# Optimization experiments

Hardware: AMD Instinct MI355X
Metric: run time of the kernel (lower is better)

## Reference

```python
import jax, jax.numpy as jnp
import numpy as np

J = 24
ROOT = 0
# SMPL kinematic tree parents
PARENTS = [-1, 0, 0, 0, 1, 2, 3, 4, 5, 6, 7, 8, 9, 9, 9, 12, 13, 14, 16, 17, 18, 19, 20, 21]
RES_SCALE = 0.1


def rodrigues(rvec):
    """Axis-angle (..., 3) -> rotation matrix (..., 3, 3)."""
    theta = jnp.linalg.norm(rvec, axis=-1, keepdims=True)          # (...,1)
    axis = rvec / jnp.maximum(theta, 1e-8)
    x, y, z = axis[..., 0], axis[..., 1], axis[..., 2]
    zero = jnp.zeros_like(x)
    K = jnp.stack([zero, -z, y, z, zero, -x, -y, x, zero], axis=-1)
    K = K.reshape(rvec.shape[:-1] + (3, 3))
    s = jnp.sin(theta)[..., None]
    c = jnp.cos(theta)[..., None]
    I = jnp.eye(3, dtype=rvec.dtype)
    return I + s * K + (1.0 - c) * (K @ K)


def _make_T(R, t):
    """(B,3,3),(B,3) -> (B,4,4) homogeneous transform."""
    B = R.shape[0]
    top = jnp.concatenate([R, t[..., None]], axis=-1)              # (B,3,4)
    bottom = jnp.broadcast_to(jnp.array([0., 0., 0., 1.], R.dtype), (B, 1, 4))
    return jnp.concatenate([top, bottom], axis=-2)


def calculate_kinematic(rest_pose, rvecs, root_locs):
    """rest_pose (J,3), rvecs (B,J,3), root_locs (B,3) -> kp (B,J,3), skts (B,J,4,4).
    Sequential tree-structured chain, unrolled over the 24 joints."""
    R = rodrigues(rvecs)                                           # (B,J,3,3)
    B = rvecs.shape[0]
    l2w = [None] * J
    l2w[ROOT] = _make_T(R[:, ROOT], root_locs)
    for j in range(1, J):
        p = PARENTS[j]
        t_local = jnp.broadcast_to(rest_pose[j] - rest_pose[p], (B, 3))
        l2w[j] = l2w[p] @ _make_T(R[:, j], t_local)
    l2w = jnp.stack(l2w, axis=1)                                   # (B,J,4,4)
    kp = l2w[..., :3, 3]                                           # (B,J,3)
    # skts = inverse(l2w) = [R^T, -R^T t]
    Rt = jnp.swapaxes(l2w[..., :3, :3], -1, -2)
    t_inv = -(Rt @ kp[..., None])                                  # (B,J,3,1)
    top = jnp.concatenate([Rt, t_inv], axis=-1)                    # (B,J,3,4)
    bottom = jnp.broadcast_to(jnp.array([0., 0., 0., 1.], l2w.dtype), (B, J, 1, 4))
    skts = jnp.concatenate([top, bottom], axis=-2)                 # (B,J,4,4)
    return kp, skts


def setup_inputs() -> dict:
    key = jax.random.key(0)
    ks = jax.random.split(key, 12)
    N, NU, E, W = 131072, 16384, 16, 128
    skip = N // NU
    din, dout = J * 3 + E, J * 3 + 3
    bones = jax.random.normal(ks[0], (N, J, 3), jnp.float32) * 0.2
    pelvis_buf = jax.random.normal(ks[1], (NU, 3), jnp.float32)
    kp_idxs = jnp.arange(N, dtype=jnp.int64) // skip
    rest_pose = jax.random.normal(ks[2], (J, 3), jnp.float32) * 0.3
    rest_pose = rest_pose.at[ROOT].set(0.0)
    # kp3d root must match pelvis buffer (original asserts allclose)
    kp3d = jnp.zeros((N, J, 3), jnp.float32).at[:, ROOT].set(pelvis_buf[kp_idxs])
    emb_table = jax.random.normal(ks[3], (NU, E), jnp.float32) * 0.02
    def lin(k, fan_in, fan_out):
        lim = 1.0 / np.sqrt(fan_in)
        k1, k2 = jax.random.split(k)
        return (jax.random.uniform(k1, (fan_in, fan_out), jnp.float32, -lim, lim),
                jax.random.uniform(k2, (fan_out,), jnp.float32, -lim, lim))
    W0, b0 = lin(ks[4], din, W)
    W1, b1 = lin(ks[5], W, W)
    W2, b2 = lin(ks[6], W, W)
    W3, b3 = lin(ks[7], W, dout)
    return dict(bones=bones, kp3d=kp3d, kp_idxs=kp_idxs, emb_table=emb_table,
                pelvis_buf=pelvis_buf, rest_pose=rest_pose,
                W0=W0, b0=b0, W1=W1, b1=b1, W2=W2, b2=b2, W3=W3, b3=b3,
                N_unique=NU)


def reference(bones, kp3d, kp_idxs, emb_table, pelvis_buf, rest_pose,
              W0, b0, W1, b1, W2, b2, W3, b3, N_unique):
    N = bones.shape[0]
    skip = N // N_unique
    rvecs = bones[::skip].reshape(N_unique, J * 3)                 # (Nu, 72)
    kp_u = kp_idxs[::skip]
    embs = emb_table[kp_u]                                         # (Nu, 16)
    pelvis = pelvis_buf[kp_u]                                      # (Nu, 3)
    x = jnp.concatenate([rvecs, embs], axis=-1)
    h = jax.nn.relu(x @ W0 + b0)
    h = jax.nn.relu(h @ W1 + b1)
    h = jax.nn.relu(h @ W2 + b2)
    residual = (h @ W3 + b3) * RES_SCALE                           # (Nu, 75)
    rvecs = (rvecs + residual[:, :J * 3]).reshape(N_unique, J, 3)
    pelvis = pelvis + residual[:, J * 3:]
    kp, skts = calculate_kinematic(rest_pose, rvecs, pelvis)
    # expand unique poses back to full batch ('i s ... -> (i s) ...')
    kp = jnp.repeat(kp, skip, axis=0)                              # (N,J,3)
    skts = jnp.repeat(skts, skip, axis=0)                          # (N,J,4,4)
    rvecs = jnp.repeat(rvecs, skip, axis=0)                        # (N,J,3)
    return kp, skts, rvecs
```

## Files before the change

kernel.cpp:

```cpp
#include <hip/hip_runtime.h>
#include <hip/hip_bf16.h>

typedef unsigned short u16;
using f32x4 = __attribute__((ext_vector_type(4))) float;
using s16x8 = __attribute__((ext_vector_type(8))) short;
using u32x4 = __attribute__((ext_vector_type(4))) unsigned int;

#define JNT 24
#define STRX 104
#define STRH 136

__device__ __forceinline__ u16 f2bf(float f) {
    unsigned int x; __builtin_memcpy(&x, &f, 4);
    unsigned int lsb = (x >> 16) & 1u;
    x += 0x7fffu + lsb;
    return (u16)(x >> 16);
}

__global__ void prep_weights(const float* __restrict__ W0, const float* __restrict__ W1,
                             const float* __restrict__ W2, const float* __restrict__ W3,
                             u16* __restrict__ wst) {
    int i = blockIdx.x * 256 + threadIdx.x;
    if (i < 12288) { int n = i / 96, k = i - n * 96; wst[i] = (k < 88) ? f2bf(W0[k * 128 + n]) : (u16)0; return; }
    i -= 12288;
    if (i < 16384) { int n = i >> 7, k = i & 127; wst[12288 + i] = f2bf(W1[k * 128 + n]); return; }
    i -= 16384;
    if (i < 16384) { int n = i >> 7, k = i & 127; wst[28672 + i] = f2bf(W2[k * 128 + n]); return; }
    i -= 16384;
    if (i < 10240) { int n = i >> 7, k = i & 127; wst[45056 + i] = (n < 75) ? f2bf(W3[k * 75 + n]) : (u16)0; }
}

template<int BASE, int CNT>
__device__ __forceinline__ void mlp_l3(const u16* __restrict__ H, const u16* __restrict__ W3t,
                                       const float* __restrict__ b3, float* __restrict__ res_s,
                                       int lr, int lk, int drow) {
    f32x4 acc[CNT];
#pragma unroll
    for (int t = 0; t < CNT; ++t) {
        int col = (BASE + t) * 16 + lr;
        float bv = (col < 75) ? b3[col] : 0.f;
        acc[t] = (f32x4){bv, bv, bv, bv};
    }
#pragma unroll
    for (int ks = 0; ks < 4; ++ks) {
        s16x8 a = *(const s16x8*)&H[lr * STRH + ks * 32 + lk];
#pragma unroll
        for (int t = 0; t < CNT; ++t) {
            s16x8 b = *(const s16x8*)&W3t[((BASE + t) * 16 + lr) * 128 + ks * 32 + lk];
            acc[t] = __builtin_amdgcn_mfma_f32_16x16x32_bf16(a, b, acc[t], 0, 0, 0);
        }
    }
#pragma unroll
    for (int t = 0; t < CNT; ++t) {
        int col = (BASE + t) * 16 + lr;
        if (col < 75) {
#pragma unroll
            for (int q = 0; q < 4; ++q)
                res_s[(drow + q) * 80 + col] = acc[t][q] * 0.1f;
        }
    }
}

__device__ const int KPARP[32] = {0,0,0,0,1,2,3,4,5,6,7,8,9,9,9,12,13,14,16,17,18,19,20,21,0,0,0,0,0,0,0,0};
__device__ const int KDEPP[32] = {0,1,1,1,2,2,2,3,3,3,4,4,4,4,4,5,5,5,6,6,7,7,8,8,99,99,99,99,99,99,99,99};

__global__ __launch_bounds__(256, 3)
void fused_kernel(const float* __restrict__ bones, const float* __restrict__ emb,
                  const float* __restrict__ pelvis, const float* __restrict__ rest,
                  const float* __restrict__ b0, const float* __restrict__ b1,
                  const float* __restrict__ b2, const float* __restrict__ b3,
                  const u16* __restrict__ wst, float* __restrict__ out,
                  int N, int bstride) {
    __shared__ __align__(16) unsigned char smem[22016];
    float* res_s = (float*)smem;
    u16* Xs = (u16*)(smem + 5120);
    u16* H1 = (u16*)(smem + 8448);
    u16* H2 = (u16*)(smem + 12800);
    float* so8 = (float*)(smem + 5120);

    const int tid = threadIdx.x;
    const int row0 = blockIdx.x * 16;

    for (int i = tid; i < 16 * 96; i += 256) {
        int r = i / 96, c = i - r * 96;
        int u = row0 + r;
        float v = 0.f;
        if (c < 72)      v = bones[(size_t)u * bstride + c];
        else if (c < 88) v = emb[(size_t)u * 16 + (c - 72)];
        Xs[r * STRX + c] = f2bf(v);
    }
    __syncthreads();

    const int lane = tid & 63;
    const int wave = tid >> 6;
    const int lr = lane & 15;
    const int lk = (lane >> 4) * 8;
    const int drow = (lane >> 4) * 4;
    const u16* W0t = wst;
    const u16* W1t = wst + 12288;
    const u16* W2t = wst + 28672;
    const u16* W3t = wst + 45056;

    {
        f32x4 acc[2];
#pragma unroll
        for (int t = 0; t < 2; ++t) { float bv = b0[(wave * 2 + t) * 16 + lr]; acc[t] = (f32x4){bv, bv, bv, bv}; }
#pragma unroll
        for (int ks = 0; ks < 3; ++ks) {
            s16x8 a = *(const s16x8*)&Xs[lr * STRX + ks * 32 + lk];
#pragma unroll
            for (int t = 0; t < 2; ++t) {
                s16x8 b = *(const s16x8*)&W0t[((wave * 2 + t) * 16 + lr) * 96 + ks * 32 + lk];
                acc[t] = __builtin_amdgcn_mfma_f32_16x16x32_bf16(a, b, acc[t], 0, 0, 0);
            }
        }
#pragma unroll
        for (int t = 0; t < 2; ++t)
#pragma unroll
            for (int q = 0; q < 4; ++q)
                H1[(drow + q) * STRH + (wave * 2 + t) * 16 + lr] = f2bf(fmaxf(acc[t][q], 0.f));
    }
    __syncthreads();
    {
        f32x4 acc[2];
#pragma unroll
        for (int t = 0; t < 2; ++t) { float bv = b1[(wave * 2 + t) * 16 + lr]; acc[t] = (f32x4){bv, bv, bv, bv}; }
#pragma unroll
        for (int ks = 0; ks < 4; ++ks) {
            s16x8 a = *(const s16x8*)&H1[lr * STRH + ks * 32 + lk];
#pragma unroll
            for (int t = 0; t < 2; ++t) {
                s16x8 b = *(const s16x8*)&W1t[((wave * 2 + t) * 16 + lr) * 128 + ks * 32 + lk];
                acc[t] = __builtin_amdgcn_mfma_f32_16x16x32_bf16(a, b, acc[t], 0, 0, 0);
            }
        }
#pragma unroll
        for (int t = 0; t < 2; ++t)
#pragma unroll
            for (int q = 0; q < 4; ++q)
                H2[(drow + q) * STRH + (wave * 2 + t) * 16 + lr] = f2bf(fmaxf(acc[t][q], 0.f));
    }
    __syncthreads();
    {
        f32x4 acc[2];
#pragma unroll
        for (int t = 0; t < 2; ++t) { float bv = b2[(wave * 2 + t) * 16 + lr]; acc[t] = (f32x4){bv, bv, bv, bv}; }
#pragma unroll
        for (int ks = 0; ks < 4; ++ks) {
            s16x8 a = *(const s16x8*)&H2[lr * STRH + ks * 32 + lk];
#pragma unroll
            for (int t = 0; t < 2; ++t) {
                s16x8 b = *(const s16x8*)&W2t[((wave * 2 + t) * 16 + lr) * 128 + ks * 32 + lk];
                acc[t] = __builtin_amdgcn_mfma_f32_16x16x32_bf16(a, b, acc[t], 0, 0, 0);
            }
        }
        __syncthreads();
#pragma unroll
        for (int t = 0; t < 2; ++t)
#pragma unroll
            for (int q = 0; q < 4; ++q)
                H1[(drow + q) * STRH + (wave * 2 + t) * 16 + lr] = f2bf(fmaxf(acc[t][q], 0.f));
    }
    __syncthreads();
    if      (wave == 0) mlp_l3<0, 2>(H1, W3t, b3, res_s, lr, lk, drow);
    else if (wave == 1) mlp_l3<2, 1>(H1, W3t, b3, res_s, lr, lk, drow);
    else if (wave == 2) mlp_l3<3, 1>(H1, W3t, b3, res_s, lr, lk, drow);
    else                mlp_l3<4, 1>(H1, W3t, b3, res_s, lr, lk, drow);
    __syncthreads();

    const int half = lane >> 5, j = lane & 31;
    const int par = KPARP[j], dep = KDEPP[j];
    const int plane = (lane & 32) | par;

    const u32x4* ls = (const u32x4*)so8;
    u32x4* o4 = (u32x4*)out;
    const size_t r1 = (size_t)N * 18;
    const size_t r2 = (size_t)N * 114;

    for (int pass = 0; pass < 2; ++pass) {
        const int sloc8 = wave * 2 + half;
        const int sl = pass * 8 + sloc8;
        const size_t u = (size_t)row0 + sl;

        float R[3][3] = {{1.f,0.f,0.f},{0.f,1.f,0.f},{0.f,0.f,1.f}};
        float T[3] = {0.f, 0.f, 0.f};
        float rv0 = 0.f, rv1 = 0.f, rv2 = 0.f;

        if (j < JNT) {
            const float* rs = &res_s[sl * 80];
            const float* bn = &bones[u * (size_t)bstride];
            rv0 = bn[j * 3 + 0] + rs[j * 3 + 0];
            rv1 = bn[j * 3 + 1] + rs[j * 3 + 1];
            rv2 = bn[j * 3 + 2] + rs[j * 3 + 2];
            float th = sqrtf(rv0 * rv0 + rv1 * rv1 + rv2 * rv2);
            float s = sinf(th), c = cosf(th);
            float inv = 1.f / fmaxf(th, 1e-8f);
            float ax = rv0 * inv, ay = rv1 * inv, az = rv2 * inv;
            float K[3][3] = {{0.f, -az, ay}, {az, 0.f, -ax}, {-ay, ax, 0.f}};
            float KK[3][3];
#pragma unroll
            for (int r = 0; r < 3; ++r)
#pragma unroll
                for (int cc = 0; cc < 3; ++cc)
                    KK[r][cc] = K[r][0] * K[0][cc] + K[r][1] * K[1][cc] + K[r][2] * K[2][cc];
            float omc = 1.f - c;
#pragma unroll
            for (int r = 0; r < 3; ++r)
#pragma unroll
                for (int cc = 0; cc < 3; ++cc)
                    R[r][cc] = ((r == cc) ? 1.f : 0.f) + s * K[r][cc] + omc * KK[r][cc];
            if (j == 0) {
#pragma unroll
                for (int cc = 0; cc < 3; ++cc) T[cc] = pelvis[u * 3 + cc] + rs[72 + cc];
            } else {
#pragma unroll
                for (int cc = 0; cc < 3; ++cc) T[cc] = rest[j * 3 + cc] - rest[par * 3 + cc];
            }
        }

        for (int lev = 1; lev <= 8; ++lev) {
            float p00 = __shfl(R[0][0], plane), p01 = __shfl(R[0][1], plane), p02 = __shfl(R[0][2], plane);
            float p10 = __shfl(R[1][0], plane), p11 = __shfl(R[1][1], plane), p12 = __shfl(R[1][2], plane);
            float p20 = __shfl(R[2][0], plane), p21 = __shfl(R[2][1], plane), p22 = __shfl(R[2][2], plane);
            float q0  = __shfl(T[0],   plane), q1  = __shfl(T[1],   plane), q2  = __shfl(T[2],   plane);
            if (dep == lev) {
                float n00 = p00 * R[0][0] + p01 * R[1][0] + p02 * R[2][0];
                float n01 = p00 * R[0][1] + p01 * R[1][1] + p02 * R[2][1];
                float n02 = p00 * R[0][2] + p01 * R[1][2] + p02 * R[2][2];
                float n10 = p10 * R[0][0] + p11 * R[1][0] + p12 * R[2][0];
                float n11 = p10 * R[0][1] + p11 * R[1][1] + p12 * R[2][1];
                float n12 = p10 * R[0][2] + p11 * R[1][2] + p12 * R[2][2];
                float n20 = p20 * R[0][0] + p21 * R[1][0] + p22 * R[2][0];
                float n21 = p20 * R[0][1] + p21 * R[1][1] + p22 * R[2][1];
                float n22 = p20 * R[0][2] + p21 * R[1][2] + p22 * R[2][2];
                float m0  = p00 * T[0] + p01 * T[1] + p02 * T[2] + q0;
                float m1  = p10 * T[0] + p11 * T[1] + p12 * T[2] + q1;
                float m2  = p20 * T[0] + p21 * T[1] + p22 * T[2] + q2;
                R[0][0] = n00; R[0][1] = n01; R[0][2] = n02;
                R[1][0] = n10; R[1][1] = n11; R[1][2] = n12;
                R[2][0] = n20; R[2][1] = n21; R[2][2] = n22;
                T[0] = m0; T[1] = m1; T[2] = m2;
            }
        }

        if (j < JNT) {
            float* kp = &so8[sloc8 * 528 + j * 3];
            kp[0] = T[0]; kp[1] = T[1]; kp[2] = T[2];
            float* sk = &so8[sloc8 * 528 + 72 + j * 16];
#pragma unroll
            for (int r = 0; r < 3; ++r) {
                sk[r * 4 + 0] = R[0][r];
                sk[r * 4 + 1] = R[1][r];
                sk[r * 4 + 2] = R[2][r];
                sk[r * 4 + 3] = -(R[0][r] * T[0] + R[1][r] * T[1] + R[2][r] * T[2]);
            }
            sk[12] = 0.f; sk[13] = 0.f; sk[14] = 0.f; sk[15] = 1.0f;
            float* rv = &so8[sloc8 * 528 + 456 + j * 3];
            rv[0] = rv0; rv[1] = rv1; rv[2] = rv2;
        }
        __syncthreads();

        for (int i = tid; i < 8 * 1056; i += 256) {
            int s = i / 1056, w = i - s * 1056;
            size_t uu = (size_t)row0 + pass * 8 + s;
            const u32x4* src; size_t dst;
            if (w < 144)      { src = ls + s * 132 + (w % 18);              dst = uu * 144 + w; }
            else if (w < 912) { int w2 = w - 144;
                                src = ls + s * 132 + 18 + (w2 % 96);        dst = r1 + uu * 768 + w2; }
            else              { int w3 = w - 912;
                                src = ls + s * 132 + 114 + (w3 % 18);       dst = r2 + uu * 144 + w3; }
            o4[dst] = *src;
        }
        __syncthreads();
    }
}

extern "C" void kernel_launch(void* const* d_in, const int* in_sizes, int n_in,
                              void* d_out, int out_size, void* d_ws, size_t ws_size,
                              hipStream_t stream) {
    const float* bones  = (const float*)d_in[0];
    const float* emb    = (const float*)d_in[3];
    const float* pelvis = (const float*)d_in[4];
    const float* rest   = (const float*)d_in[5];
    const float* W0 = (const float*)d_in[6];
    const float* b0 = (const float*)d_in[7];
    const float* W1 = (const float*)d_in[8];
    const float* b1 = (const float*)d_in[9];
    const float* W2 = (const float*)d_in[10];
    const float* b2 = (const float*)d_in[11];
    const float* W3 = (const float*)d_in[12];
    const float* b3 = (const float*)d_in[13];

    const int N    = in_sizes[0] / 72;
    const int NU   = in_sizes[3] / 16;
    const int skip = N / NU;
    const int bstride = skip * 72;

    u16* wst = (u16*)d_ws;

    prep_weights<<<216, 256, 0, stream>>>(W0, W1, W2, W3, wst);
    fused_kernel<<<NU / 16, 256, 0, stream>>>(bones, emb, pelvis, rest,
                                              b0, b1, b2, b3, wst,
                                              (float*)d_out, N, bstride);
}
```

Baseline: 70.73 us.

## Warp-specialize kinematics: producer waves compute while consumer waves stream outputs

Splits the kinematic-chain epilogue into four passes of four samples. Waves 0-1 compute transforms into alternating shared buffers while waves 2-3 write the previous pass's results to global memory, so compute and stores overlap. The skinning-matrix rows are now written to shared memory as 16-byte vector stores. The cost is that only half the waves compute at a time, and the final pass is drained by all threads after the loop, which could lengthen the critical path.

```diff
diff --git a/kernel.cpp b/kernel.cpp
--- a/kernel.cpp
+++ b/kernel.cpp
@@ -76,7 +76,8 @@
     u16* Xs = (u16*)(smem + 5120);
     u16* H1 = (u16*)(smem + 8448);
     u16* H2 = (u16*)(smem + 12800);
-    float* so8 = (float*)(smem + 5120);
+    float* bufA = (float*)(smem + 5120);
+    float* bufB = (float*)(smem + 13568);
 
     const int tid = threadIdx.x;
     const int row0 = blockIdx.x * 16;
@@ -171,108 +172,117 @@
     const int half = lane >> 5, j = lane & 31;
     const int par = KPARP[j], dep = KDEPP[j];
     const int plane = (lane & 32) | par;
-
-    const u32x4* ls = (const u32x4*)so8;
+    const bool producer = (wave < 2);
+
     u32x4* o4 = (u32x4*)out;
     const size_t r1 = (size_t)N * 18;
     const size_t r2 = (size_t)N * 114;
 
-    for (int pass = 0; pass < 2; ++pass) {
-        const int sloc8 = wave * 2 + half;
-        const int sl = pass * 8 + sloc8;
-        const size_t u = (size_t)row0 + sl;
-
-        float R[3][3] = {{1.f,0.f,0.f},{0.f,1.f,0.f},{0.f,0.f,1.f}};
-        float T[3] = {0.f, 0.f, 0.f};
-        float rv0 = 0.f, rv1 = 0.f, rv2 = 0.f;
-
-        if (j < JNT) {
-            const float* rs = &res_s[sl * 80];
-            const float* bn = &bones[u * (size_t)bstride];
-            rv0 = bn[j * 3 + 0] + rs[j * 3 + 0];
-            rv1 = bn[j * 3 + 1] + rs[j * 3 + 1];
-            rv2 = bn[j * 3 + 2] + rs[j * 3 + 2];
-            float th = sqrtf(rv0 * rv0 + rv1 * rv1 + rv2 * rv2);
-            float s = sinf(th), c = cosf(th);
-            float inv = 1.f / fmaxf(th, 1e-8f);
-            float ax = rv0 * inv, ay = rv1 * inv, az = rv2 * inv;
-            float K[3][3] = {{0.f, -az, ay}, {az, 0.f, -ax}, {-ay, ax, 0.f}};
-            float KK[3][3];
-#pragma unroll
-            for (int r = 0; r < 3; ++r)
-#pragma unroll
-                for (int cc = 0; cc < 3; ++cc)
-                    KK[r][cc] = K[r][0] * K[0][cc] + K[r][1] * K[1][cc] + K[r][2] * K[2][cc];
-            float omc = 1.f - c;
-#pragma unroll
-            for (int r = 0; r < 3; ++r)
-#pragma unroll
-                for (int cc = 0; cc < 3; ++cc)
-                    R[r][cc] = ((r == cc) ? 1.f : 0.f) + s * K[r][cc] + omc * KK[r][cc];
-            if (j == 0) {
-#pragma unroll
-                for (int cc = 0; cc < 3; ++cc) T[cc] = pelvis[u * 3 + cc] + rs[72 + cc];
-            } else {
-#pragma unroll
-                for (int cc = 0; cc < 3; ++cc) T[cc] = rest[j * 3 + cc] - rest[par * 3 + cc];
-            }
-        }
-
-        for (int lev = 1; lev <= 8; ++lev) {
-            float p00 = __shfl(R[0][0], plane), p01 = __shfl(R[0][1], plane), p02 = __shfl(R[0][2], plane);
-            float p10 = __shfl(R[1][0], plane), p11 = __shfl(R[1][1], plane), p12 = __shfl(R[1][2], plane);
-            float p20 = __shfl(R[2][0], plane), p21 = __shfl(R[2][1], plane), p22 = __shfl(R[2][2], plane);
-            float q0  = __shfl(T[0],   plane), q1  = __shfl(T[1],   plane), q2  = __shfl(T[2],   plane);
-            if (dep == lev) {
-                float n00 = p00 * R[0][0] + p01 * R[1][0] + p02 * R[2][0];
-                float n01 = p00 * R[0][1] + p01 * R[1][1] + p02 * R[2][1];
-                float n02 = p00 * R[0][2] + p01 * R[1][2] + p02 * R[2][2];
-                float n10 = p10 * R[0][0] + p11 * R[1][0] + p12 * R[2][0];
-                float n11 = p10 * R[0][1] + p11 * R[1][1] + p12 * R[2][1];
-                float n12 = p10 * R[0][2] + p11 * R[1][2] + p12 * R[2][2];
-                float n20 = p20 * R[0][0] + p21 * R[1][0] + p22 * R[2][0];
-                float n21 = p20 * R[0][1] + p21 * R[1][1] + p22 * R[2][1];
-                float n22 = p20 * R[0][2] + p21 * R[1][2] + p22 * R[2][2];
-                float m0  = p00 * T[0] + p01 * T[1] + p02 * T[2] + q0;
-                float m1  = p10 * T[0] + p11 * T[1] + p12 * T[2] + q1;
-                float m2  = p20 * T[0] + p21 * T[1] + p22 * T[2] + q2;
-                R[0][0] = n00; R[0][1] = n01; R[0][2] = n02;
-                R[1][0] = n10; R[1][1] = n11; R[1][2] = n12;
-                R[2][0] = n20; R[2][1] = n21; R[2][2] = n22;
-                T[0] = m0; T[1] = m1; T[2] = m2;
-            }
-        }
-
-        if (j < JNT) {
-            float* kp = &so8[sloc8 * 528 + j * 3];
-            kp[0] = T[0]; kp[1] = T[1]; kp[2] = T[2];
-            float* sk = &so8[sloc8 * 528 + 72 + j * 16];
-#pragma unroll
-            for (int r = 0; r < 3; ++r) {
-                sk[r * 4 + 0] = R[0][r];
-                sk[r * 4 + 1] = R[1][r];
-                sk[r * 4 + 2] = R[2][r];
-                sk[r * 4 + 3] = -(R[0][r] * T[0] + R[1][r] * T[1] + R[2][r] * T[2]);
-            }
-            sk[12] = 0.f; sk[13] = 0.f; sk[14] = 0.f; sk[15] = 1.0f;
-            float* rv = &so8[sloc8 * 528 + 456 + j * 3];
-            rv[0] = rv0; rv[1] = rv1; rv[2] = rv2;
+#define WRITE4(base_s, buf, T0, STRIDE)                                                \
+    {                                                                                  \
+        const u32x4* ls = (const u32x4*)(buf);                                         \
+        for (int i = (T0); i < 4 * 1056; i += (STRIDE)) {                              \
+            int s = i / 1056, w = i - s * 1056;                                        \
+            size_t uu = (size_t)row0 + (base_s) + s;                                   \
+            const u32x4* src; size_t dst;                                              \
+            if (w < 144)      { src = ls + s * 132 + (w % 18);        dst = uu * 144 + w; }       \
+            else if (w < 912) { int w2 = w - 144;                                      \
+                                src = ls + s * 132 + 18 + (w2 % 96);  dst = r1 + uu * 768 + w2; } \
+            else              { int w3 = w - 912;                                      \
+                                src = ls + s * 132 + 114 + (w3 % 18); dst = r2 + uu * 144 + w3; } \
+            o4[dst] = *src;                                                            \
+        }                                                                              \
+    }
+
+    for (int p = 0; p < 4; ++p) {
+        if (producer) {
+            float* sbuf = (p & 1) ? bufB : bufA;
+            const int sloc4 = wave * 2 + half;
+            const int sl = p * 4 + sloc4;
+            const size_t u = (size_t)row0 + sl;
+
+            float R[3][3] = {{1.f,0.f,0.f},{0.f,1.f,0.f},{0.f,0.f,1.f}};
+            float T[3] = {0.f, 0.f, 0.f};
+            float rv0 = 0.f, rv1 = 0.f, rv2 = 0.f;
+
+            if (j < JNT) {
+                const float* rs = &res_s[sl * 80];
+                const float* bn = &bones[u * (size_t)bstride];
+                rv0 = bn[j * 3 + 0] + rs[j * 3 + 0];
+                rv1 = bn[j * 3 + 1] + rs[j * 3 + 1];
+                rv2 = bn[j * 3 + 2] + rs[j * 3 + 2];
+                float th = sqrtf(rv0 * rv0 + rv1 * rv1 + rv2 * rv2);
+                float s = sinf(th), c = cosf(th);
+                float inv = 1.f / fmaxf(th, 1e-8f);
+                float ax = rv0 * inv, ay = rv1 * inv, az = rv2 * inv;
+                float K[3][3] = {{0.f, -az, ay}, {az, 0.f, -ax}, {-ay, ax, 0.f}};
+                float KK[3][3];
+#pragma unroll
+                for (int r = 0; r < 3; ++r)
+#pragma unroll
+                    for (int cc = 0; cc < 3; ++cc)
+                        KK[r][cc] = K[r][0] * K[0][cc] + K[r][1] * K[1][cc] + K[r][2] * K[2][cc];
+                float omc = 1.f - c;
+#pragma unroll
+                for (int r = 0; r < 3; ++r)
+#pragma unroll
+                    for (int cc = 0; cc < 3; ++cc)
+                        R[r][cc] = ((r == cc) ? 1.f : 0.f) + s * K[r][cc] + omc * KK[r][cc];
+                if (j == 0) {
+#pragma unroll
+                    for (int cc = 0; cc < 3; ++cc) T[cc] = pelvis[u * 3 + cc] + rs[72 + cc];
+                } else {
+#pragma unroll
+                    for (int cc = 0; cc < 3; ++cc) T[cc] = rest[j * 3 + cc] - rest[par * 3 + cc];
+                }
+            }
+
+            for (int lev = 1; lev <= 8; ++lev) {
+                float p00 = __shfl(R[0][0], plane), p01 = __shfl(R[0][1], plane), p02 = __shfl(R[0][2], plane);
+                float p10 = __shfl(R[1][0], plane), p11 = __shfl(R[1][1], plane), p12 = __shfl(R[1][2], plane);
+                float p20 = __shfl(R[2][0], plane), p21 = __shfl(R[2][1], plane), p22 = __shfl(R[2][2], plane);
+                float q0  = __shfl(T[0],   plane), q1  = __shfl(T[1],   plane), q2  = __shfl(T[2],   plane);
+                if (dep == lev) {
+                    float n00 = p00 * R[0][0] + p01 * R[1][0] + p02 * R[2][0];
+                    float n01 = p00 * R[0][1] + p01 * R[1][1] + p02 * R[2][1];
+                    float n02 = p00 * R[0][2] + p01 * R[1][2] + p02 * R[2][2];
+                    float n10 = p10 * R[0][0] + p11 * R[1][0] + p12 * R[2][0];
+                    float n11 = p10 * R[0][1] + p11 * R[1][1] + p12 * R[2][1];
+                    float n12 = p10 * R[0][2] + p11 * R[1][2] + p12 * R[2][2];
+                    float n20 = p20 * R[0][0] + p21 * R[1][0] + p22 * R[2][0];
+                    float n21 = p20 * R[0][1] + p21 * R[1][1] + p22 * R[2][1];
+                    float n22 = p20 * R[0][2] + p21 * R[1][2] + p22 * R[2][2];
+                    float m0  = p00 * T[0] + p01 * T[1] + p02 * T[2] + q0;
+                    float m1  = p10 * T[0] + p11 * T[1] + p12 * T[2] + q1;
+                    float m2  = p20 * T[0] + p21 * T[1] + p22 * T[2] + q2;
+                    R[0][0] = n00; R[0][1] = n01; R[0][2] = n02;
+                    R[1][0] = n10; R[1][1] = n11; R[1][2] = n12;
+                    R[2][0] = n20; R[2][1] = n21; R[2][2] = n22;
+                    T[0] = m0; T[1] = m1; T[2] = m2;
+                }
+            }
+
+            if (j < JNT) {
+                float* kp = &sbuf[sloc4 * 528 + j * 3];
+                kp[0] = T[0]; kp[1] = T[1]; kp[2] = T[2];
+                f32x4* sk4 = (f32x4*)&sbuf[sloc4 * 528 + 72 + j * 16];
+#pragma unroll
+                for (int r = 0; r < 3; ++r) {
+                    float ti = -(R[0][r] * T[0] + R[1][r] * T[1] + R[2][r] * T[2]);
+                    sk4[r] = (f32x4){R[0][r], R[1][r], R[2][r], ti};
+                }
+                sk4[3] = (f32x4){0.f, 0.f, 0.f, 1.f};
+                float* rv = &sbuf[sloc4 * 528 + 456 + j * 3];
+                rv[0] = rv0; rv[1] = rv1; rv[2] = rv2;
+            }
+        } else if (p >= 1) {
+            const float* wb = ((p - 1) & 1) ? bufB : bufA;
+            WRITE4((p - 1) * 4, wb, tid - 128, 128);
         }
         __syncthreads();
-
-        for (int i = tid; i < 8 * 1056; i += 256) {
-            int s = i / 1056, w = i - s * 1056;
-            size_t uu = (size_t)row0 + pass * 8 + s;
-            const u32x4* src; size_t dst;
-            if (w < 144)      { src = ls + s * 132 + (w % 18);              dst = uu * 144 + w; }
-            else if (w < 912) { int w2 = w - 144;
-                                src = ls + s * 132 + 18 + (w2 % 96);        dst = r1 + uu * 768 + w2; }
-            else              { int w3 = w - 912;
-                                src = ls + s * 132 + 114 + (w3 % 18);       dst = r2 + uu * 144 + w3; }
-            o4[dst] = *src;
-        }
-        __syncthreads();
-    }
+    }
+    WRITE4(12, bufB, tid, 256);
+#undef WRITE4
 }
 
 extern "C" void kernel_launch(void* const* d_in, const int* in_sizes, int n_in,
```

Result: no change. 71.27 us (+0.8%).
